# Performance work log

Measured on AMD Instinct MI355X. Metric: run time of the kernel, lower is better.

## Reference

```python
import jax, jax.numpy as jnp
import numpy as np

FEAT = 256
HEADS = 8
HD = FEAT // HEADS
POS = 128
NEG = 128
H = 128
W = 128
B = 8
NSLOT = 512
LN_EPS = 1e-5


def setup_inputs() -> dict:
    key = jax.random.key(0)
    ks = jax.random.split(key, 8)
    HW = H * W
    features = jax.random.normal(ks[0], (HW, B, FEAT), dtype=jnp.float32)
    pos_encodings = jax.random.normal(ks[1], (HW, B, FEAT), dtype=jnp.float32)
    slots = jax.random.normal(ks[2], (1, NSLOT, FEAT), dtype=jnp.float32)
    curio_maps = jax.random.uniform(ks[3], (NSLOT, H, W), dtype=jnp.float32)
    batch_idx = jax.random.randint(ks[4], (NSLOT,), 0, B, dtype=jnp.int32)
    # parameters (xavier-ish scale)
    in_proj_weight = jax.random.normal(ks[5], (3 * FEAT, FEAT), dtype=jnp.float32) * 0.05
    in_proj_bias = jnp.zeros((3 * FEAT,), dtype=jnp.float32)
    out_w = jax.random.normal(ks[6], (FEAT, FEAT), dtype=jnp.float32) * 0.05
    out_b = jnp.zeros((FEAT,), dtype=jnp.float32)
    ln_g = jnp.ones((FEAT,), dtype=jnp.float32)
    ln_b = jnp.zeros((FEAT,), dtype=jnp.float32)
    return {
        'slots': slots, 'features': features, 'pos_encodings': pos_encodings,
        'curio_maps': curio_maps, 'batch_idx': batch_idx,
        'in_proj_weight': in_proj_weight, 'in_proj_bias': in_proj_bias,
        'out_w': out_w, 'out_b': out_b, 'ln_g': ln_g, 'ln_b': ln_b,
        'max_mask_entries': 0,
    }


def _sample_feat_idx(curio_maps, max_mask_entries):
    # curio_maps: [NSLOT, H, W] -> feat_idx: [POS+NEG, NSLOT]
    HW = curio_maps.shape[1] * curio_maps.shape[2]
    flat = curio_maps.reshape(NSLOT, HW)
    sorted_idx = jnp.argsort(-flat, axis=1)  # descending
    pos_idx = sorted_idx[:, :POS]
    pool = sorted_idx[:, POS:HW - max_mask_entries] if max_mask_entries > 0 else sorted_idx[:, POS:]
    # deterministic stand-in for random.sample: evenly-strided negatives
    stride = pool.shape[1] // NEG
    neg_idx = pool[:, ::stride][:, :NEG]
    return jnp.concatenate([pos_idx, neg_idx], axis=1).T  # [S, NSLOT]


def _forward(slots, features, pos_encodings, curio_maps, batch_idx,
             in_proj_weight, in_proj_bias, out_w, out_b, ln_g, ln_b,
             max_mask_entries):
    feat_idx = _sample_feat_idx(curio_maps, max_mask_entries)  # [S, NSLOT]
    S = feat_idx.shape[0]
    qw, kw, vw = in_proj_weight[:FEAT], in_proj_weight[FEAT:2 * FEAT], in_proj_weight[2 * FEAT:]
    qb, kb, vb = in_proj_bias[:FEAT], in_proj_bias[FEAT:2 * FEAT], in_proj_bias[2 * FEAT:]
    scaling = float(HD) ** -0.5
    # sample_type == 'after': project full maps, then gather
    q = (jnp.einsum('bnf,gf->bng', slots, qw) + qb) * scaling       # [1, NSLOT, FEAT]
    k = jnp.einsum('pbf,gf->pbg', features + pos_encodings, kw) + kb  # [HW, B, FEAT]
    v = jnp.einsum('pbf,gf->pbg', features, vw) + vb                  # [HW, B, FEAT]
    kg = k[feat_idx, batch_idx[None, :], :]            # [S, NSLOT, FEAT]
    vg = v[feat_idx[:POS], batch_idx[None, :], :]      # [POS, NSLOT, FEAT]
    qh = q.reshape(NSLOT, HEADS, HD)
    kh = kg.reshape(S, NSLOT, HEADS, HD)
    vh = vg.reshape(POS, NSLOT, HEADS, HD)
    affinities = jnp.einsum('nhd,snhd->snh', qh, kh)   # [S, NSLOT, HEADS]
    attn = jax.nn.softmax(affinities[:POS], axis=0)    # softmax over positive samples
    attn_out = jnp.einsum('pnh,pnhd->nhd', attn, vh).reshape(1, NSLOT, FEAT)
    attn_out = jnp.einsum('bnf,gf->bng', attn_out, out_w) + out_b
    x = slots + attn_out  # dropout is identity in eval
    mu = jnp.mean(x, axis=-1, keepdims=True)
    var = jnp.var(x, axis=-1, keepdims=True)
    new_slots = (x - mu) / jnp.sqrt(var + LN_EPS) * ln_g + ln_b
    return new_slots, affinities


def reference(slots, features, pos_encodings, curio_maps, batch_idx,
              in_proj_weight, in_proj_bias, out_w, out_b, ln_g, ln_b,
              max_mask_entries):
    return _forward(slots, features, pos_encodings, curio_maps, batch_idx,
                    in_proj_weight, in_proj_bias, out_w, out_b, ln_g, ln_b,
                    max_mask_entries)
```

## Files before the change

kernel.cpp:

```cpp
#include <hip/hip_runtime.h>
#include <hip/hip_bf16.h>

#define FEAT 256
#define HEADS 8
#define HD 32
#define POSN 128
#define NEGN 128
#define HWN 16384
#define BN 8
#define NSLOT 512
#define S_TOT 256
#define LN_EPS 1e-5f
#define NBKT 4096
#define AFF_OFF (NSLOT*FEAT)

typedef float f32x4 __attribute__((ext_vector_type(4)));

__device__ __forceinline__ unsigned short bf16r(float x) {
    unsigned int u = __float_as_uint(x);
    u += 0x7FFFu + ((u >> 16) & 1u);
    return (unsigned short)(u >> 16);
}
__device__ __forceinline__ float bf16f(unsigned short h) {
    return __uint_as_float((unsigned int)h << 16);
}

__device__ __forceinline__ float dot8w(const float* __restrict__ Wrows,
                                       f32x4 x, int e0, int e1, int e2, int lane)
{
    const float* p = Wrows + 4 * lane;
    f32x4 w0 = *(const f32x4*)(p + 0*FEAT);
    f32x4 w1 = *(const f32x4*)(p + 1*FEAT);
    f32x4 w2 = *(const f32x4*)(p + 2*FEAT);
    f32x4 w3 = *(const f32x4*)(p + 3*FEAT);
    f32x4 w4 = *(const f32x4*)(p + 4*FEAT);
    f32x4 w5 = *(const f32x4*)(p + 5*FEAT);
    f32x4 w6 = *(const f32x4*)(p + 6*FEAT);
    f32x4 w7 = *(const f32x4*)(p + 7*FEAT);
    float p0 = x[0]*w0[0] + x[1]*w0[1] + x[2]*w0[2] + x[3]*w0[3];
    float p1 = x[0]*w1[0] + x[1]*w1[1] + x[2]*w1[2] + x[3]*w1[3];
    float p2 = x[0]*w2[0] + x[1]*w2[1] + x[2]*w2[2] + x[3]*w2[3];
    float p3 = x[0]*w3[0] + x[1]*w3[1] + x[2]*w3[2] + x[3]*w3[3];
    float p4 = x[0]*w4[0] + x[1]*w4[1] + x[2]*w4[2] + x[3]*w4[3];
    float p5 = x[0]*w5[0] + x[1]*w5[1] + x[2]*w5[2] + x[3]*w5[3];
    float p6 = x[0]*w6[0] + x[1]*w6[1] + x[2]*w6[2] + x[3]*w6[3];
    float p7 = x[0]*w7[0] + x[1]*w7[1] + x[2]*w7[2] + x[3]*w7[3];
    float s0 = e0 ? p0 : p1, s1 = e0 ? p2 : p3, s2 = e0 ? p4 : p5, s3 = e0 ? p6 : p7;
    float a0 = (e0 ? p1 : p0) + __shfl_xor(s0, 1);
    float a1 = (e0 ? p3 : p2) + __shfl_xor(s1, 1);
    float a2 = (e0 ? p5 : p4) + __shfl_xor(s2, 1);
    float a3 = (e0 ? p7 : p6) + __shfl_xor(s3, 1);
    float u0 = e1 ? a0 : a1, u1 = e1 ? a2 : a3;
    float c0 = (e1 ? a1 : a0) + __shfl_xor(u0, 2);
    float c1 = (e1 ? a3 : a2) + __shfl_xor(u1, 2);
    float u2 = e2 ? c0 : c1;
    float d = (e2 ? c1 : c0) + __shfl_xor(u2, 4);
    d += __shfl_xor(d, 8);
    d += __shfl_xor(d, 16);
    d += __shfl_xor(d, 32);
    return d;
}

__global__ __launch_bounds__(256) void k_sample_qkw(const float* __restrict__ curio,
                                                    const int* __restrict__ mme_p,
                                                    const float* __restrict__ slots,
                                                    const float* __restrict__ ipw,
                                                    const float* __restrict__ ipb,
                                                    int* __restrict__ fi_t,
                                                    float* __restrict__ qkw,
                                                    float* __restrict__ qkb)
{
    __shared__ unsigned int hist[NBKT];
    __shared__ uint16_t offs[NBKT];
    __shared__ uint16_t sidx[HWN];
    __shared__ unsigned int ssum[256];
    __shared__ float srow[FEAT];
    __shared__ float qrow[FEAT];
    int slot = blockIdx.x, t = threadIdx.x;
    int lane = t & 63, w = t >> 6;
    const float* cm = curio + (size_t)slot * HWN;
    const f32x4* cm4 = (const f32x4*)cm;

    for (int i = t; i < NBKT; i += 256) hist[i] = 0;
    __syncthreads();

    unsigned int bkA[16], bkB[16];
#pragma unroll
    for (int j = 0; j < 16; j++) {
        f32x4 v = cm4[j * 256 + t];
        int b0 = (int)(v[0] * 4096.0f); b0 = b0 < 0 ? 0 : (b0 > NBKT-1 ? NBKT-1 : b0);
        int b1 = (int)(v[1] * 4096.0f); b1 = b1 < 0 ? 0 : (b1 > NBKT-1 ? NBKT-1 : b1);
        int b2 = (int)(v[2] * 4096.0f); b2 = b2 < 0 ? 0 : (b2 > NBKT-1 ? NBKT-1 : b2);
        int b3 = (int)(v[3] * 4096.0f); b3 = b3 < 0 ? 0 : (b3 > NBKT-1 ? NBKT-1 : b3);
        bkA[j] = (unsigned int)b0 | ((unsigned int)b1 << 16);
        bkB[j] = (unsigned int)b2 | ((unsigned int)b3 << 16);
        atomicAdd(&hist[b0], 1u); atomicAdd(&hist[b1], 1u);
        atomicAdd(&hist[b2], 1u); atomicAdd(&hist[b3], 1u);
    }
    __syncthreads();

    unsigned int lsum = 0;
    int base = t * 16;
    for (int j = 0; j < 16; j++) lsum += hist[NBKT-1 - (base + j)];
    ssum[t] = lsum; __syncthreads();
    for (int off = 1; off < 256; off <<= 1) {
        unsigned int v = (t >= off) ? ssum[t - off] : 0u;
        __syncthreads();
        ssum[t] += v;
        __syncthreads();
    }
    unsigned int run = ssum[t] - lsum;
    for (int j = 0; j < 16; j++) {
        int b = NBKT-1 - (base + j);
        offs[b] = (uint16_t)run;
        run += hist[b];
    }
    __syncthreads();
    for (int i = t; i < NBKT; i += 256) hist[i] = 0;
    __syncthreads();

#pragma unroll
    for (int j = 0; j < 16; j++) {
        int idx0 = (j * 256 + t) * 4;
        int b0 = (int)(bkA[j] & 0xFFFFu), b1 = (int)(bkA[j] >> 16);
        int b2 = (int)(bkB[j] & 0xFFFFu), b3 = (int)(bkB[j] >> 16);
        unsigned int p0 = (unsigned int)offs[b0] + atomicAdd(&hist[b0], 1u);
        sidx[p0] = (uint16_t)(idx0 + 0);
        unsigned int p1 = (unsigned int)offs[b1] + atomicAdd(&hist[b1], 1u);
        sidx[p1] = (uint16_t)(idx0 + 1);
        unsigned int p2 = (unsigned int)offs[b2] + atomicAdd(&hist[b2], 1u);
        sidx[p2] = (uint16_t)(idx0 + 2);
        unsigned int p3 = (unsigned int)offs[b3] + atomicAdd(&hist[b3], 1u);
        sidx[p3] = (uint16_t)(idx0 + 3);
    }
    __syncthreads();

    int mme = mme_p[0];
    int stride = (HWN - POSN - mme) / NEGN;
    int r = (t < POSN) ? t : (POSN + stride * (t - POSN));
    int lo = 0, hi = NBKT - 1;
    while (lo < hi) { int mid = (lo + hi) >> 1; if ((int)offs[mid] <= r) hi = mid; else lo = mid + 1; }
    int bkt = lo;
    int start = (int)offs[bkt];
    int cnt   = (int)hist[bkt];
    int rr = r - start;
    int besti = sidx[start + (rr < cnt ? rr : 0)];
    for (int j = 0; j < cnt; j++) {
        int ij = sidx[start + j];
        float vj = cm[ij];
        int rank = 0;
        for (int j2 = 0; j2 < cnt; j2++) {
            int i2 = sidx[start + j2];
            float v2 = cm[i2];
            if (v2 > vj || (v2 == vj && i2 < ij)) rank++;
        }
        if (rank == rr) { besti = ij; break; }
    }
    fi_t[slot * S_TOT + t] = besti;

    __syncthreads();
    srow[t] = slots[slot * FEAT + t];
    __syncthreads();
    {
        int e0 = lane & 1, e1 = (lane >> 1) & 1, e2 = (lane >> 2) & 1;
        f32x4 xs = *(const f32x4*)&srow[4 * lane];
        const float scaling = 0.17677669529663687f;
#pragma unroll
        for (int c = 0; c < 8; c++) {
            int r0 = w * 64 + c * 8;
            float d = dot8w(ipw + (size_t)r0 * FEAT, xs, e0, e1, e2, lane);
            if (lane < 8) qrow[r0 + lane] = (d + ipb[r0 + lane]) * scaling;
        }
    }
    __syncthreads();
    if (t < HEADS) {
        float s = 0.f;
        for (int d = 0; d < HD; d++) s += qrow[t*HD + d] * ipb[FEAT + t*HD + d];
        qkb[slot * HEADS + t] = s;
    }
    const float* kw = ipw + FEAT * FEAT;
    for (int e = t; e < HEADS * FEAT; e += 256) {
        int h = e >> 8, f = e & 255;
        float s = 0.f;
#pragma unroll
        for (int d = 0; d < HD; d++) s += qrow[h*HD + d] * kw[(h*HD + d) * FEAT + f];
        qkw[(size_t)slot * (HEADS*FEAT) + e] = s;
    }
}

__global__ __launch_bounds__(512) void k_attn(const float* __restrict__ features,
                                              const float* __restrict__ pos_enc,
                                              const int* __restrict__ batch_idx,
                                              const int* __restrict__ fi_t,
                                              const float* __restrict__ qkw,
                                              const float* __restrict__ qkb,
                                              const float* __restrict__ slots,
                                              const float* __restrict__ ipw,
                                              const float* __restrict__ ipb,
                                              const float* __restrict__ out_w,
                                              const float* __restrict__ out_b,
                                              const float* __restrict__ ln_g,
                                              const float* __restrict__ ln_b,
                                              float* __restrict__ aff_out,
                                              float* __restrict__ out)
{
    __shared__ int   fi_l[S_TOT];
    __shared__ float qkb_l[HEADS];
    __shared__ __align__(16) float affP[POSN][8];
    __shared__ f32x4 wfp[4][HEADS][64];
    __shared__ __align__(16) float ao_l[FEAT];
    __shared__ float xgh[FEAT];
    __shared__ float rr12[8];

    int n = blockIdx.x, t = threadIdx.x, lane = t & 63, w = t >> 6;
    if (t < S_TOT) fi_l[t] = fi_t[n * S_TOT + t];
    if (t < HEADS) qkb_l[t] = qkb[n * HEADS + t];
    int b = batch_idx[n];

    const float* qk = qkw + (size_t)n * (HEADS*FEAT) + 4 * lane;
    f32x4 qw0 = *(const f32x4*)(qk + 0*FEAT);
    f32x4 qw1 = *(const f32x4*)(qk + 1*FEAT);
    f32x4 qw2 = *(const f32x4*)(qk + 2*FEAT);
    f32x4 qw3 = *(const f32x4*)(qk + 3*FEAT);
    f32x4 qw4 = *(const f32x4*)(qk + 4*FEAT);
    f32x4 qw5 = *(const f32x4*)(qk + 5*FEAT);
    f32x4 qw6 = *(const f32x4*)(qk + 6*FEAT);
    f32x4 qw7 = *(const f32x4*)(qk + 7*FEAT);
    __syncthreads();
    float qb = qkb_l[lane & 7];
    int e0 = lane & 1, e1 = (lane >> 1) & 1, e2 = (lane >> 2) & 1;

    auto dorow = [&](int p, f32x4 x, bool toLds) {
        float p0 = x[0]*qw0[0] + x[1]*qw0[1] + x[2]*qw0[2] + x[3]*qw0[3];
        float p1 = x[0]*qw1[0] + x[1]*qw1[1] + x[2]*qw1[2] + x[3]*qw1[3];
        float p2 = x[0]*qw2[0] + x[1]*qw2[1] + x[2]*qw2[2] + x[3]*qw2[3];
        float p3 = x[0]*qw3[0] + x[1]*qw3[1] + x[2]*qw3[2] + x[3]*qw3[3];
        float p4 = x[0]*qw4[0] + x[1]*qw4[1] + x[2]*qw4[2] + x[3]*qw4[3];
        float p5 = x[0]*qw5[0] + x[1]*qw5[1] + x[2]*qw5[2] + x[3]*qw5[3];
        float p6 = x[0]*qw6[0] + x[1]*qw6[1] + x[2]*qw6[2] + x[3]*qw6[3];
        float p7 = x[0]*qw7[0] + x[1]*qw7[1] + x[2]*qw7[2] + x[3]*qw7[3];
        float s0 = e0 ? p0 : p1, s1 = e0 ? p2 : p3, s2 = e0 ? p4 : p5, s3 = e0 ? p6 : p7;
        float a0 = (e0 ? p1 : p0) + __shfl_xor(s0, 1);
        float a1 = (e0 ? p3 : p2) + __shfl_xor(s1, 1);
        float a2 = (e0 ? p5 : p4) + __shfl_xor(s2, 1);
        float a3 = (e0 ? p7 : p6) + __shfl_xor(s3, 1);
        float u0 = e1 ? a0 : a1, u1 = e1 ? a2 : a3;
        float c0 = (e1 ? a1 : a0) + __shfl_xor(u0, 2);
        float c1 = (e1 ? a3 : a2) + __shfl_xor(u1, 2);
        float u2 = e2 ? c0 : c1;
        float d = (e2 ? c1 : c0) + __shfl_xor(u2, 4);
        d += __shfl_xor(d, 8);
        d += __shfl_xor(d, 16);
        d += __shfl_xor(d, 32);
        d += qb;
        if (lane < 8) {
            aff_out[(size_t)p * (NSLOT*HEADS) + n*HEADS + lane] = d;
            if (toLds) affP[p][lane] = d;
        }
    };

    auto rowaddr = [&](int s) {
        return ((size_t)fi_l[s] * BN + b) * FEAT + 4 * lane;
    };

    ushort4 cache[16];
    {
        size_t aA = rowaddr(w);
        size_t aB = rowaddr(w + 8);
        f32x4 fA = *(const f32x4*)(features + aA), gA = *(const f32x4*)(pos_enc + aA);
        f32x4 fB = *(const f32x4*)(features + aB), gB = *(const f32x4*)(pos_enc + aB);
#pragma unroll
        for (int i = 0; i < 16; i += 2) {
            f32x4 cf = fA, cg = gA;
            if (i + 2 < 16) {
                size_t nb = rowaddr(w + 8*(i+2));
                fA = *(const f32x4*)(features + nb); gA = *(const f32x4*)(pos_enc + nb);
            }
            { ushort4 pk; pk.x = bf16r(cf[0]); pk.y = bf16r(cf[1]);
              pk.z = bf16r(cf[2]); pk.w = bf16r(cf[3]); cache[i] = pk; }
            dorow(w + 8*i, cf + cg, true);
            f32x4 cf2 = fB, cg2 = gB;
            if (i + 3 < 16) {
                size_t nb = rowaddr(w + 8*(i+3));
                fB = *(const f32x4*)(features + nb); gB = *(const f32x4*)(pos_enc + nb);
            }
            { ushort4 pk; pk.x = bf16r(cf2[0]); pk.y = bf16r(cf2[1]);
              pk.z = bf16r(cf2[2]); pk.w = bf16r(cf2[3]); cache[i+1] = pk; }
            dorow(w + 8*(i+1), cf2 + cg2, true);
        }
    }

    f32x4 fA, gA, fB, gB;
    {
        size_t aA = rowaddr(POSN + w);
        size_t aB = rowaddr(POSN + w + 8);
        fA = *(const f32x4*)(features + aA); gA = *(const f32x4*)(pos_enc + aA);
        fB = *(const f32x4*)(features + aB); gB = *(const f32x4*)(pos_enc + aB);
    }
    __syncthreads();

    if (t < 256) {
        int h = t >> 5, l = t & 31;
        float v0 = affP[l][h], v1 = affP[l+32][h], v2 = affP[l+64][h], v3 = affP[l+96][h];
        float m = fmaxf(fmaxf(v0, v1), fmaxf(v2, v3));
        for (int off = 16; off > 0; off >>= 1) m = fmaxf(m, __shfl_xor(m, off, 32));
        float ex0 = expf(v0 - m), ex1 = expf(v1 - m), ex2 = expf(v2 - m), ex3 = expf(v3 - m);
        float s = ex0 + ex1 + ex2 + ex3;
        for (int off = 16; off > 0; off >>= 1) s += __shfl_xor(s, off, 32);
        float inv = 1.0f / s;
        affP[l][h] = ex0*inv; affP[l+32][h] = ex1*inv; affP[l+64][h] = ex2*inv; affP[l+96][h] = ex3*inv;
    }
    __syncthreads();

    f32x4 acc[8];
#pragma unroll
    for (int h = 0; h < 8; h++) acc[h] = (f32x4){0.f,0.f,0.f,0.f};
    {
        auto wstep = [&](int i) {
            int p = w + 8*i;
            ushort4 pk = cache[i];
            f32x4 xf;
            xf[0] = bf16f(pk.x); xf[1] = bf16f(pk.y);
            xf[2] = bf16f(pk.z); xf[3] = bf16f(pk.w);
            const f32x4* ap = (const f32x4*)&affP[p][0];
            f32x4 a03 = ap[0], a47 = ap[1];
            acc[0] += xf * a03[0];
            acc[1] += xf * a03[1];
            acc[2] += xf * a03[2];
            acc[3] += xf * a03[3];
            acc[4] += xf * a47[0];
            acc[5] += xf * a47[1];
            acc[6] += xf * a47[2];
            acc[7] += xf * a47[3];
        };
#pragma unroll
        for (int i = 0; i < 16; i += 2) {
            f32x4 cf = fA, cg = gA;
            if (i + 2 < 16) {
                size_t nb = rowaddr(POSN + w + 8*(i+2));
                fA = *(const f32x4*)(features + nb); gA = *(const f32x4*)(pos_enc + nb);
            }
            wstep(i);
            dorow(POSN + w + 8*i, cf + cg, false);
            f32x4 cf2 = fB, cg2 = gB;
            if (i + 3 < 16) {
                size_t nb = rowaddr(POSN + w + 8*(i+3));
                fB = *(const f32x4*)(features + nb); gB = *(const f32x4*)(pos_enc + nb);
            }
            wstep(i+1);
            dorow(POSN + w + 8*(i+1), cf2 + cg2, false);
        }
    }
    if (w < 4) {
#pragma unroll
        for (int h = 0; h < 8; h++) wfp[w][h][lane] = acc[h];
    }
    __syncthreads();
    if (w >= 4) {
#pragma unroll
        for (int h = 0; h < 8; h++) wfp[w-4][h][lane] += acc[h];
    }
    __syncthreads();
    {
        int h = t >> 6, q2 = t & 63;
        f32x4 s = wfp[0][h][q2] + wfp[1][h][q2] + wfp[2][h][q2] + wfp[3][h][q2];
        wfp[0][h][q2] = s;
    }
    __syncthreads();

    {
        const float* vw = ipw + (size_t)(2*FEAT) * FEAT;
        f32x4 xv = wfp[0][w][lane];
#pragma unroll
        for (int c = 0; c < 4; c++) {
            int r0 = w * 32 + c * 8;
            float d = dot8w(vw + (size_t)r0 * FEAT, xv, e0, e1, e2, lane);
            if (lane < 8) ao_l[r0 + lane] = d + ipb[2*FEAT + r0 + lane];
        }
    }
    __syncthreads();

    {
        f32x4 xo = *(const f32x4*)&ao_l[4 * lane];
#pragma unroll
        for (int c = 0; c < 4; c++) {
            int r0 = w * 32 + c * 8;
            float d = dot8w(out_w + (size_t)r0 * FEAT, xo, e0, e1, e2, lane);
            if (lane < 8) xgh[r0 + lane] = d;
        }
    }
    __syncthreads();

    float xg = 0.f;
    if (t < 256) {
        xg = xgh[t] + out_b[t] + slots[n * FEAT + t];
        float s1 = xg, s2 = xg * xg;
        for (int off = 32; off > 0; off >>= 1) {
            s1 += __shfl_xor(s1, off);
            s2 += __shfl_xor(s2, off);
        }
        if ((t & 63) == 0) { rr12[t >> 6] = s1; rr12[4 + (t >> 6)] = s2; }
    }
    __syncthreads();
    if (t < 256) {
        float sum1 = rr12[0] + rr12[1] + rr12[2] + rr12[3];
        float sum2 = rr12[4] + rr12[5] + rr12[6] + rr12[7];
        float mu  = sum1 * (1.0f / FEAT);
        float var = sum2 * (1.0f / FEAT) - mu * mu;
        float nrm = (xg - mu) * rsqrtf(var + LN_EPS);
        out[n * FEAT + t] = nrm * ln_g[t] + ln_b[t];
    }
}

extern "C" void kernel_launch(void* const* d_in, const int* in_sizes, int n_in,
                              void* d_out, int out_size, void* d_ws, size_t ws_size,
                              hipStream_t stream)
{
    (void)in_sizes; (void)n_in; (void)out_size; (void)ws_size;
    const float* slots    = (const float*)d_in[0];
    const float* features = (const float*)d_in[1];
    const float* pos_enc  = (const float*)d_in[2];
    const float* curio    = (const float*)d_in[3];
    const int*   batch_idx= (const int*)d_in[4];
    const float* ipw      = (const float*)d_in[5];
    const float* ipb      = (const float*)d_in[6];
    const float* out_w    = (const float*)d_in[7];
    const float* out_b    = (const float*)d_in[8];
    const float* ln_g     = (const float*)d_in[9];
    const float* ln_b     = (const float*)d_in[10];
    const int*   mme      = (const int*)d_in[11];
    float* out = (float*)d_out;

    char* ws = (char*)d_ws;
    int*   fi_t = (int*)ws;
    float* qkw  = (float*)(ws + (512 << 10));
    float* qkb  = (float*)(ws + (512 << 10) + (4 << 20));
    float* aff  = out + AFF_OFF;

    hipLaunchKernelGGL(k_sample_qkw, dim3(NSLOT), dim3(256), 0, stream,
                       curio, mme, slots, ipw, ipb, fi_t, qkw, qkb);
    hipLaunchKernelGGL(k_attn, dim3(NSLOT), dim3(512), 0, stream,
                       features, pos_enc, batch_idx, fi_t, qkw, qkb, slots, ipw, ipb,
                       out_w, out_b, ln_g, ln_b, aff, out);
}
```

Measured before the change: 109.5 us.

## Defer negative-sample affinity rows into V-projection and out-projection phases

Negative-sample rows 8–15 per wave were computed alongside the weighted-V accumulation. They are now deferred and interleaved with the V-projection and output-projection GEMV stages, with the feature and pos-encoding prefetch chain carried across the barriers. The wstep accumulations are batched four per iteration. The aim is to hide the global-load latency of the negative rows behind the serial projection work and shorten the pre-reduction loop. In exchange, more loads stay live across barriers, which may raise register pressure.

```diff
diff --git a/kernel.cpp b/kernel.cpp
--- a/kernel.cpp
+++ b/kernel.cpp
@@ -334,23 +334,24 @@
             acc[7] += xf * a47[3];
         };
 #pragma unroll
-        for (int i = 0; i < 16; i += 2) {
+        for (int i = 0; i < 8; i += 2) {
             f32x4 cf = fA, cg = gA;
-            if (i + 2 < 16) {
+            {
                 size_t nb = rowaddr(POSN + w + 8*(i+2));
                 fA = *(const f32x4*)(features + nb); gA = *(const f32x4*)(pos_enc + nb);
             }
-            wstep(i);
+            wstep(2*i);   wstep(2*i+1);
             dorow(POSN + w + 8*i, cf + cg, false);
             f32x4 cf2 = fB, cg2 = gB;
-            if (i + 3 < 16) {
+            {
                 size_t nb = rowaddr(POSN + w + 8*(i+3));
                 fB = *(const f32x4*)(features + nb); gB = *(const f32x4*)(pos_enc + nb);
             }
-            wstep(i+1);
+            wstep(2*i+2); wstep(2*i+3);
             dorow(POSN + w + 8*(i+1), cf2 + cg2, false);
         }
     }
+
     if (w < 4) {
 #pragma unroll
         for (int h = 0; h < 8; h++) wfp[w][h][lane] = acc[h];
@@ -372,10 +373,35 @@
         const float* vw = ipw + (size_t)(2*FEAT) * FEAT;
         f32x4 xv = wfp[0][w][lane];
 #pragma unroll
-        for (int c = 0; c < 4; c++) {
-            int r0 = w * 32 + c * 8;
-            float d = dot8w(vw + (size_t)r0 * FEAT, xv, e0, e1, e2, lane);
-            if (lane < 8) ao_l[r0 + lane] = d + ipb[2*FEAT + r0 + lane];
+        for (int c = 0; c < 4; c += 2) {
+            f32x4 cf = fA, cg = gA;
+            if (c + 2 < 4) {
+                size_t nb = rowaddr(POSN + w + 8*(10+c));
+                fA = *(const f32x4*)(features + nb); gA = *(const f32x4*)(pos_enc + nb);
+            } else {
+                size_t nb = rowaddr(POSN + w + 8*12);
+                fA = *(const f32x4*)(features + nb); gA = *(const f32x4*)(pos_enc + nb);
+            }
+            {
+                int r0 = w * 32 + c * 8;
+                float d = dot8w(vw + (size_t)r0 * FEAT, xv, e0, e1, e2, lane);
+                if (lane < 8) ao_l[r0 + lane] = d + ipb[2*FEAT + r0 + lane];
+            }
+            dorow(POSN + w + 8*(8+c), cf + cg, false);
+            f32x4 cf2 = fB, cg2 = gB;
+            if (c + 2 < 4) {
+                size_t nb = rowaddr(POSN + w + 8*(11+c));
+                fB = *(const f32x4*)(features + nb); gB = *(const f32x4*)(pos_enc + nb);
+            } else {
+                size_t nb = rowaddr(POSN + w + 8*13);
+                fB = *(const f32x4*)(features + nb); gB = *(const f32x4*)(pos_enc + nb);
+            }
+            {
+                int r0 = w * 32 + (c+1) * 8;
+                float d = dot8w(vw + (size_t)r0 * FEAT, xv, e0, e1, e2, lane);
+                if (lane < 8) ao_l[r0 + lane] = d + ipb[2*FEAT + r0 + lane];
+            }
+            dorow(POSN + w + 8*(9+c), cf2 + cg2, false);
         }
     }
     __syncthreads();
@@ -383,10 +409,29 @@
     {
         f32x4 xo = *(const f32x4*)&ao_l[4 * lane];
 #pragma unroll
-        for (int c = 0; c < 4; c++) {
-            int r0 = w * 32 + c * 8;
-            float d = dot8w(out_w + (size_t)r0 * FEAT, xo, e0, e1, e2, lane);
-            if (lane < 8) xgh[r0 + lane] = d;
+        for (int c = 0; c < 4; c += 2) {
+            f32x4 cf = fA, cg = gA;
+            if (c + 2 < 4) {
+                size_t nb = rowaddr(POSN + w + 8*14);
+                fA = *(const f32x4*)(features + nb); gA = *(const f32x4*)(pos_enc + nb);
+            }
+            {
+                int r0 = w * 32 + c * 8;
+                float d = dot8w(out_w + (size_t)r0 * FEAT, xo, e0, e1, e2, lane);
+                if (lane < 8) xgh[r0 + lane] = d;
+            }
+            dorow(POSN + w + 8*(12+c), cf + cg, false);
+            f32x4 cf2 = fB, cg2 = gB;
+            if (c + 2 < 4) {
+                size_t nb = rowaddr(POSN + w + 8*15);
+                fB = *(const f32x4*)(features + nb); gB = *(const f32x4*)(pos_enc + nb);
+            }
+            {
+                int r0 = w * 32 + (c+1) * 8;
+                float d = dot8w(out_w + (size_t)r0 * FEAT, xo, e0, e1, e2, lane);
+                if (lane < 8) xgh[r0 + lane] = d;
+            }
+            dorow(POSN + w + 8*(13+c), cf2 + cg2, false);
         }
     }
     __syncthreads();
```

Measured after the change: 131.0 us. +19.6%, slower.

## Overlap last negative-row affinity work with V projection across warp halves

Applied to the files above, without the earlier changes.

The main loop now handles only the first 96 negative rows, while the last 32 negative rows are moved to warps 4-7. Those warps compute them at the same time as warps 0-3 run the V-projection matvec, with each of warps 0-3 covering two heads. The goal is to fill the phase where previously every warp did the V projection with otherwise idle time, shortening the critical path. The cost is load imbalance between the two warp halves and a dependency on the rowaddr and dorow indexing staying correct for the remapped rows.

```diff
diff --git a/kernel.cpp b/kernel.cpp
--- a/kernel.cpp
+++ b/kernel.cpp
@@ -334,23 +334,25 @@
             acc[7] += xf * a47[3];
         };
 #pragma unroll
-        for (int i = 0; i < 16; i += 2) {
+        for (int i = 0; i < 12; i += 2) {
             f32x4 cf = fA, cg = gA;
-            if (i + 2 < 16) {
+            if (i + 2 < 12) {
                 size_t nb = rowaddr(POSN + w + 8*(i+2));
                 fA = *(const f32x4*)(features + nb); gA = *(const f32x4*)(pos_enc + nb);
             }
             wstep(i);
             dorow(POSN + w + 8*i, cf + cg, false);
             f32x4 cf2 = fB, cg2 = gB;
-            if (i + 3 < 16) {
+            if (i + 3 < 12) {
                 size_t nb = rowaddr(POSN + w + 8*(i+3));
                 fB = *(const f32x4*)(features + nb); gB = *(const f32x4*)(pos_enc + nb);
             }
             wstep(i+1);
             dorow(POSN + w + 8*(i+1), cf2 + cg2, false);
         }
-    }
+        wstep(12); wstep(13); wstep(14); wstep(15);
+    }
+
     if (w < 4) {
 #pragma unroll
         for (int h = 0; h < 8; h++) wfp[w][h][lane] = acc[h];
@@ -368,14 +370,39 @@
     }
     __syncthreads();
 
-    {
+    if (w < 4) {
         const float* vw = ipw + (size_t)(2*FEAT) * FEAT;
-        f32x4 xv = wfp[0][w][lane];
-#pragma unroll
-        for (int c = 0; c < 4; c++) {
-            int r0 = w * 32 + c * 8;
-            float d = dot8w(vw + (size_t)r0 * FEAT, xv, e0, e1, e2, lane);
-            if (lane < 8) ao_l[r0 + lane] = d + ipb[2*FEAT + r0 + lane];
+#pragma unroll
+        for (int hh = 0; hh < 2; hh++) {
+            int h = 2*w + hh;
+            f32x4 xv = wfp[0][h][lane];
+#pragma unroll
+            for (int c = 0; c < 4; c++) {
+                int r0 = h * 32 + c * 8;
+                float d = dot8w(vw + (size_t)r0 * FEAT, xv, e0, e1, e2, lane);
+                if (lane < 8) ao_l[r0 + lane] = d + ipb[2*FEAT + r0 + lane];
+            }
+        }
+    } else {
+        int base = POSN + 96 + (w - 4) * 8;
+        size_t aA = rowaddr(base);
+        size_t aB = rowaddr(base + 1);
+        f32x4 nfA = *(const f32x4*)(features + aA), ngA = *(const f32x4*)(pos_enc + aA);
+        f32x4 nfB = *(const f32x4*)(features + aB), ngB = *(const f32x4*)(pos_enc + aB);
+#pragma unroll
+        for (int j = 0; j < 8; j += 2) {
+            f32x4 cf = nfA, cg = ngA;
+            if (j + 2 < 8) {
+                size_t nb = rowaddr(base + j + 2);
+                nfA = *(const f32x4*)(features + nb); ngA = *(const f32x4*)(pos_enc + nb);
+            }
+            dorow(base + j, cf + cg, false);
+            f32x4 cf2 = nfB, cg2 = ngB;
+            if (j + 3 < 8) {
+                size_t nb = rowaddr(base + j + 3);
+                nfB = *(const f32x4*)(features + nb); ngB = *(const f32x4*)(pos_enc + nb);
+            }
+            dorow(base + j + 1, cf2 + cg2, false);
         }
     }
     __syncthreads();
```

Result: no change. 110.5 us (+0.9%).
